# Optimization experiments

Hardware: AMD Instinct MI355X
Metric: run time of the kernel (lower is better)

The kernel has to match this reference:

```python
import jax, jax.numpy as jnp
import numpy as np

N_NODES = 10000
N_EDGES = 640000
D_FEAT = 128


def setup_inputs() -> dict:
    key = jax.random.key(0)
    k1, k2, k3 = jax.random.split(key, 3)
    feat = jax.random.normal(k1, (N_NODES, D_FEAT), dtype=jnp.float32)
    src = jax.random.randint(k2, (N_EDGES,), 0, N_NODES, dtype=jnp.int64)
    dst = jax.random.randint(k3, (N_EDGES,), 0, N_NODES, dtype=jnp.int64)
    beta = jnp.ones((1,), dtype=jnp.float32)
    return {"feat": feat, "src": src, "dst": dst, "beta": beta}


def reference(feat, src, dst, beta):
    # L2-normalize node features along feature dim (eps matches torch F.normalize)
    norm = feat / jnp.maximum(jnp.linalg.norm(feat, axis=-1, keepdims=True), 1e-12)
    # per-edge cosine similarity: sum over d of norm[src] * norm[dst]  -> [E]
    cos = jnp.einsum('ed,ed->e', norm[src], norm[dst])
    e = beta[0] * cos
    # edge softmax segmented over destination nodes
    seg_max = jax.ops.segment_max(e, dst, num_segments=N_NODES)  # [N]
    ex = jnp.exp(e - seg_max[dst])                               # [E]
    seg_sum = jax.ops.segment_sum(ex, dst, num_segments=N_NODES)  # [N]
    p = ex / seg_sum[dst]                                        # [E]
    # weighted neighbor aggregation: sum_e p_e * feat[src_e] into dst
    msg = feat[src] * p[:, None]                                 # [E, d]
    out = jax.ops.segment_sum(msg, dst, num_segments=N_NODES)    # [N, d]
    return out
```

## Files before the change

### kernel.cpp

```cpp
#include <hip/hip_runtime.h>
#include <math.h>

#define D_FEAT 128
#define EPB_SHIFT 13
#define EPB 8192
#define N_NODES_MAX 10016
#define CAP 128

#define DPP_XOR1 0xB1
#define DPP_XOR2 0x4E
#define DPP_HALF_MIRROR 0x141
#define DPP_MIRROR      0x140

__device__ __forceinline__ unsigned short f2bf(float x) {
    unsigned int b = __float_as_uint(x);
    return (unsigned short)((b + 0x7fffu + ((b >> 16) & 1u)) >> 16);
}
__device__ __forceinline__ float2 bf2_to_f2(unsigned int u) {
    return make_float2(__uint_as_float(u << 16), __uint_as_float(u & 0xffff0000u));
}
template <int CTRL>
__device__ __forceinline__ float dpp_add(float x) {
    int t = __builtin_amdgcn_update_dpp(__float_as_int(x), __float_as_int(x),
                                        CTRL, 0xF, 0xF, false);
    return x + __int_as_float(t);
}

__global__ __launch_bounds__(1024) void hist_norm_kernel(
        const float* __restrict__ feat,
        const int* __restrict__ dst,
        unsigned int* __restrict__ nfb,
        float* __restrict__ invn,
        int* __restrict__ hist,
        unsigned short* __restrict__ lrank,
        int n_nodes, int n_edges, int nbh) {
    __shared__ int lhist[N_NODES_MAX];
    int tid = (int)threadIdx.x;
    if ((int)blockIdx.x < nbh) {
        int b = blockIdx.x;
        for (int i = tid; i < n_nodes; i += 1024) lhist[i] = 0;
        __syncthreads();
        int e0 = b << EPB_SHIFT;
        int e1 = e0 + EPB;
        if (e1 > n_edges) e1 = n_edges;
        for (int e = e0 + tid; e < e1; e += 1024) {
            int d = dst[e];
            lrank[e] = (unsigned short)atomicAdd(&lhist[d], 1);
        }
        __syncthreads();
        for (int i = tid; i < n_nodes; i += 1024)
            hist[b * n_nodes + i] = lhist[i];
    } else {
        int node = ((int)blockIdx.x - nbh) * 16 + (tid >> 6);
        int lane = tid & 63;
        if (node >= n_nodes) return;
        float2 f = ((const float2*)feat)[node * 64 + lane];
        float ss = f.x * f.x + f.y * f.y;
        #pragma unroll
        for (int off = 1; off < 64; off <<= 1)
            ss += __shfl_xor(ss, off, 64);
        unsigned int lo = f2bf(f.x), hi = f2bf(f.y);
        nfb[node * 64 + lane] = (hi << 16) | lo;
        if (lane == 0) invn[node] = 1.0f / fmaxf(sqrtf(ss), 1e-12f);
    }
}

__global__ __launch_bounds__(256) void scan_kernel(int* __restrict__ hist,
                                                   int* __restrict__ cnt,
                                                   int n_nodes, int nbh) {
    int node = (int)(blockIdx.x * blockDim.x + threadIdx.x);
    if (node >= n_nodes) return;
    int base = 0;
    #pragma unroll 8
    for (int b = 0; b < nbh; ++b) {
        int idx = b * n_nodes + node;
        int v = hist[idx];
        hist[idx] = base;
        base += v;
    }
    cnt[node] = base;
}

__global__ __launch_bounds__(256) void scatter_kernel(
        const int* __restrict__ src,
        const int* __restrict__ dst,
        const int* __restrict__ hist,
        const unsigned short* __restrict__ lrank,
        unsigned short* __restrict__ src_sorted,
        int n_nodes, int n_edges) {
    int e = blockIdx.x * blockDim.x + threadIdx.x;
    if (e >= n_edges) return;
    int d = dst[e];
    int b = e >> EPB_SHIFT;
    int r = hist[b * n_nodes + d] + (int)lrank[e];
    if (r < CAP)
        src_sorted[((size_t)d << 7) + r] = (unsigned short)src[e];
}

__global__ void agg_kernel(const unsigned int* __restrict__ nfb,
                           const float* __restrict__ invn,
                           const float* __restrict__ beta,
                           const int* __restrict__ cnt,
                           const unsigned short* __restrict__ src_sorted,
                           float* __restrict__ out, int n_nodes) {
    __shared__ float sA[2][16][8];
    __shared__ float sL[2];
    int tid  = (int)threadIdx.x;
    int gw   = ((int)blockIdx.x * 256 + tid) >> 6;
    int node = gw >> 1;
    int w    = gw & 1;
    int pair = tid >> 7;
    int lane = tid & 63;
    int q  = lane >> 4;
    int ql = lane & 15;

    int deg = cnt[node];
    if (deg > CAP) deg = CAP;
    int h = (((deg + 1) >> 1) + 3) & ~3;
    if (h > deg) h = deg;
    int start = w ? h : 0;
    int mycnt = w ? (deg - h) : h;
    int beg = (node << 7) + start;

    float bd = beta[0] * invn[node];

    uint4 du = ((const uint4*)nfb)[(size_t)node * 16 + ql];
    float2 d0 = bf2_to_f2(du.x), d1 = bf2_to_f2(du.y);
    float2 d2 = bf2_to_f2(du.z), d3 = bf2_to_f2(du.w);

    float l = 0.0f;
    float a0 = 0.f, a1 = 0.f, a2 = 0.f, a3 = 0.f;
    float a4 = 0.f, a5 = 0.f, a6 = 0.f, a7 = 0.f;

    {
        bool valid = lane < mycnt;
        int gi = beg + lane;
        int idx = valid ? (int)src_sorted[gi] : 0;
        float ivm = valid ? invn[idx] * bd : 0.0f;

        #pragma unroll 8
        for (int j = 0; j < mycnt; j += 4) {
            int jj = j + q;
            int   sj  = __shfl(idx, jj, 64);
            float inj = __shfl(ivm, jj, 64);
            uint4 u = ((const uint4*)nfb)[(size_t)sj * 16 + ql];
            float2 f0 = bf2_to_f2(u.x), f1 = bf2_to_f2(u.y);
            float2 f2 = bf2_to_f2(u.z), f3 = bf2_to_f2(u.w);
            float part = f0.x * d0.x + f0.y * d0.y + f1.x * d1.x + f1.y * d1.y
                       + f2.x * d2.x + f2.y * d2.y + f3.x * d3.x + f3.y * d3.y;
            part = dpp_add<DPP_XOR1>(part);
            part = dpp_add<DPP_XOR2>(part);
            part = dpp_add<DPP_HALF_MIRROR>(part);
            part = dpp_add<DPP_MIRROR>(part);
            float w_ = __expf(part * inj);
            w_ = (jj < mycnt) ? w_ : 0.0f;
            l += w_;
            a0 += w_ * f0.x;  a1 += w_ * f0.y;
            a2 += w_ * f1.x;  a3 += w_ * f1.y;
            a4 += w_ * f2.x;  a5 += w_ * f2.y;
            a6 += w_ * f3.x;  a7 += w_ * f3.y;
        }
    }
    #pragma unroll
    for (int off = 1; off < 64; off <<= 1)
        l += __shfl_xor(l, off, 64);
    a0 += __shfl_xor(a0, 16, 64); a0 += __shfl_xor(a0, 32, 64);
    a1 += __shfl_xor(a1, 16, 64); a1 += __shfl_xor(a1, 32, 64);
    a2 += __shfl_xor(a2, 16, 64); a2 += __shfl_xor(a2, 32, 64);
    a3 += __shfl_xor(a3, 16, 64); a3 += __shfl_xor(a3, 32, 64);
    a4 += __shfl_xor(a4, 16, 64); a4 += __shfl_xor(a4, 32, 64);
    a5 += __shfl_xor(a5, 16, 64); a5 += __shfl_xor(a5, 32, 64);
    a6 += __shfl_xor(a6, 16, 64); a6 += __shfl_xor(a6, 32, 64);
    a7 += __shfl_xor(a7, 16, 64); a7 += __shfl_xor(a7, 32, 64);

    if (w == 1 && q == 0) {
        sA[pair][ql][0] = a0; sA[pair][ql][1] = a1;
        sA[pair][ql][2] = a2; sA[pair][ql][3] = a3;
        sA[pair][ql][4] = a4; sA[pair][ql][5] = a5;
        sA[pair][ql][6] = a6; sA[pair][ql][7] = a7;
        if (ql == 0) sL[pair] = l;
    }
    __syncthreads();
    if (w == 0 && q == 0) {
        l += sL[pair];
        a0 += sA[pair][ql][0]; a1 += sA[pair][ql][1];
        a2 += sA[pair][ql][2]; a3 += sA[pair][ql][3];
        a4 += sA[pair][ql][4]; a5 += sA[pair][ql][5];
        a6 += sA[pair][ql][6]; a7 += sA[pair][ql][7];
        float invl = (l > 0.0f) ? (16.0f / l) : 0.0f;
        float4* o = (float4*)out + (size_t)node * 32 + ql * 2;
        o[0] = make_float4(a0 * invl, a1 * invl, a2 * invl, a3 * invl);
        o[1] = make_float4(a4 * invl, a5 * invl, a6 * invl, a7 * invl);
    }
}

extern "C" void kernel_launch(void* const* d_in, const int* in_sizes, int n_in,
                              void* d_out, int out_size, void* d_ws, size_t ws_size,
                              hipStream_t stream) {
    const float* feat = (const float*)d_in[0];
    const int* src    = (const int*)d_in[1];
    const int* dst    = (const int*)d_in[2];
    const float* beta = (const float*)d_in[3];
    float* out = (float*)d_out;

    const int n_nodes = in_sizes[0] / D_FEAT;
    const int n_edges = in_sizes[1];
    const int nbh = (n_edges + EPB - 1) >> EPB_SHIFT;

    char* ws = (char*)d_ws;
    size_t off = 0;
    auto alloc = [&](size_t bytes) -> void* {
        void* p = ws + off;
        off += (bytes + 255) & ~(size_t)255;
        return p;
    };
    unsigned int*   nfb        = (unsigned int*)alloc((size_t)n_nodes * 64 * 4);
    float*          invn       = (float*)alloc((size_t)n_nodes * 4);
    int*            hist       = (int*)  alloc((size_t)nbh * n_nodes * 4);
    int*            cnt        = (int*)  alloc((size_t)n_nodes * 4);
    unsigned short* lrank      = (unsigned short*)alloc((size_t)n_edges * 2);
    unsigned short* src_sorted = (unsigned short*)alloc((size_t)n_nodes * CAP * 2);

    int nb_norm = (n_nodes + 15) / 16;
    hist_norm_kernel<<<nbh + nb_norm, 1024, 0, stream>>>(
        feat, dst, nfb, invn, hist, lrank, n_nodes, n_edges, nbh);

    scan_kernel<<<(n_nodes + 255) / 256, 256, 0, stream>>>(hist, cnt, n_nodes, nbh);

    scatter_kernel<<<(n_edges + 255) / 256, 256, 0, stream>>>(
        src, dst, hist, lrank, src_sorted, n_nodes, n_edges);

    agg_kernel<<<(n_nodes * 2 + 3) / 4, 256, 0, stream>>>(
        nfb, invn, beta, cnt, src_sorted, out, n_nodes);
}
```

Measured before the change: 111.8 us.

## Fuse per-node histogram scan into scatter kernel with per-block shared prefix

Replaces the separate scan and scatter kernels with one kernel launched per edge block. Each block recomputes its own exclusive prefix over earlier blocks' histograms into shared memory, then scatters its edges using that prefix, and the last block writes the per-node counts. This removes one launch and the global read-modify-write of the histogram. The cost is redundant prefix work that grows with block index, and only nbh (79) blocks, so parallelism is low.

```diff
diff --git a/kernel.cpp b/kernel.cpp
--- a/kernel.cpp
+++ b/kernel.cpp
@@ -25,6 +25,7 @@
                                         CTRL, 0xF, 0xF, false);
     return x + __int_as_float(t);
 }
+
 
 __global__ __launch_bounds__(1024) void hist_norm_kernel(
         const float* __restrict__ feat,
@@ -65,36 +66,37 @@
     }
 }
 
-__global__ __launch_bounds__(256) void scan_kernel(int* __restrict__ hist,
-                                                   int* __restrict__ cnt,
-                                                   int n_nodes, int nbh) {
-    int node = (int)(blockIdx.x * blockDim.x + threadIdx.x);
-    if (node >= n_nodes) return;
-    int base = 0;
-    #pragma unroll 8
-    for (int b = 0; b < nbh; ++b) {
-        int idx = b * n_nodes + node;
-        int v = hist[idx];
-        hist[idx] = base;
-        base += v;
-    }
-    cnt[node] = base;
-}
-
-__global__ __launch_bounds__(256) void scatter_kernel(
+__global__ __launch_bounds__(1024) void scan_scatter_kernel(
         const int* __restrict__ src,
         const int* __restrict__ dst,
         const int* __restrict__ hist,
         const unsigned short* __restrict__ lrank,
         unsigned short* __restrict__ src_sorted,
-        int n_nodes, int n_edges) {
-    int e = blockIdx.x * blockDim.x + threadIdx.x;
-    if (e >= n_edges) return;
-    int d = dst[e];
-    int b = e >> EPB_SHIFT;
-    int r = hist[b * n_nodes + d] + (int)lrank[e];
-    if (r < CAP)
-        src_sorted[((size_t)d << 7) + r] = (unsigned short)src[e];
+        int* __restrict__ cnt,
+        int n_nodes, int n_edges, int nbh) {
+    __shared__ int pbase[N_NODES_MAX];
+    int tid = (int)threadIdx.x;
+    int b   = (int)blockIdx.x;
+
+    for (int i = tid; i < n_nodes; i += 1024) {
+        int acc = 0;
+        for (int bb = 0; bb < b; ++bb)
+            acc += hist[bb * n_nodes + i];
+        pbase[i] = acc;
+        if (b == nbh - 1)
+            cnt[i] = acc + hist[b * n_nodes + i];
+    }
+    __syncthreads();
+
+    int e0 = b << EPB_SHIFT;
+    int e1 = e0 + EPB;
+    if (e1 > n_edges) e1 = n_edges;
+    for (int e = e0 + tid; e < e1; e += 1024) {
+        int d = dst[e];
+        int r = pbase[d] + (int)lrank[e];
+        if (r < CAP)
+            src_sorted[((size_t)d << 7) + r] = (unsigned short)src[e];
+    }
 }
 
 __global__ void agg_kernel(const unsigned int* __restrict__ nfb,
@@ -225,10 +227,8 @@
     hist_norm_kernel<<<nbh + nb_norm, 1024, 0, stream>>>(
         feat, dst, nfb, invn, hist, lrank, n_nodes, n_edges, nbh);
 
-    scan_kernel<<<(n_nodes + 255) / 256, 256, 0, stream>>>(hist, cnt, n_nodes, nbh);
-
-    scatter_kernel<<<(n_edges + 255) / 256, 256, 0, stream>>>(
-        src, dst, hist, lrank, src_sorted, n_nodes, n_edges);
+    scan_scatter_kernel<<<nbh, 1024, 0, stream>>>(
+        src, dst, hist, lrank, src_sorted, cnt, n_nodes, n_edges, nbh);
 
     agg_kernel<<<(n_nodes * 2 + 3) / 4, 256, 0, stream>>>(
         nfb, invn, beta, cnt, src_sorted, out, n_nodes);
```

Result: slower. 223.9 us (+100.4%).
